# Optimization experiments

Measured on AMD Instinct MI355X. Metric: run time of the kernel, lower is better.

The kernel has to match this reference:

```python
import jax, jax.numpy as jnp
import numpy as np

N_NODES = 50000
N_EDGES = 800000
NODE_FEAT = 176
EDGE_FEAT = 4
HIDDEN = 64
LAYERS = 4
LN_EPS = 1e-5


def setup_inputs() -> dict:
    key = jax.random.key(0)
    ks = jax.random.split(key, 20)
    H, H2, Hh = HIDDEN, HIDDEN * 2, HIDDEN // 2
    inp = {
        "x": jax.random.normal(ks[0], (N_NODES, NODE_FEAT), jnp.float32),
        "edge_index": jax.random.randint(ks[1], (2, N_EDGES), 0, N_NODES, jnp.int64),
        "edge_attr": jax.random.normal(ks[2], (N_EDGES, EDGE_FEAT), jnp.float32),
        # input projection
        "in_w": jax.random.normal(ks[3], (NODE_FEAT, H), jnp.float32) * 0.05,
        "in_b": jnp.zeros((H,), jnp.float32),
        # per-layer GINEConv params (stacked over LAYERS)
        "edge_w": jax.random.normal(ks[4], (LAYERS, EDGE_FEAT, H), jnp.float32) * 0.1,
        "edge_b": jnp.zeros((LAYERS, H), jnp.float32),
        "mlp_w1": jax.random.normal(ks[5], (LAYERS, H, H2), jnp.float32) * 0.05,
        "mlp_b1": jnp.zeros((LAYERS, H2), jnp.float32),
        "mlp_w2": jax.random.normal(ks[6], (LAYERS, H2, H), jnp.float32) * 0.05,
        "mlp_b2": jnp.zeros((LAYERS, H), jnp.float32),
        "ln_g": jnp.ones((LAYERS, H), jnp.float32),
        "ln_b": jnp.zeros((LAYERS, H), jnp.float32),
        "reg_w1": jax.random.normal(ks[7], (H, Hh), jnp.float32) * 0.1,
        "reg_b1": jnp.zeros((Hh,), jnp.float32),
        "reg_w2": jax.random.normal(ks[8], (Hh, 1), jnp.float32) * 0.1,
        "reg_b2": jnp.zeros((1,), jnp.float32),
    }
    return inp


def _layernorm(z, g, b):
    mu = jnp.mean(z, axis=-1, keepdims=True)
    var = jnp.mean((z - mu) ** 2, axis=-1, keepdims=True)
    return g * (z - mu) * jax.lax.rsqrt(var + LN_EPS) + b


def reference(x, edge_index, edge_attr, in_w, in_b, edge_w, edge_b,
              mlp_w1, mlp_b1, mlp_w2, mlp_b2, ln_g, ln_b,
              reg_w1, reg_b1, reg_w2, reg_b2):
    src, dst = edge_index[0], edge_index[1]
    h = x @ in_w + in_b  # [N, H]
    for l in range(LAYERS):
        e = edge_attr @ edge_w[l] + edge_b[l]              # [E, H] edge projection
        msg = jax.nn.relu(h[src] + e)                      # gather + relu
        aggr = jax.ops.segment_sum(msg, dst, num_segments=h.shape[0])  # scatter-add
        z = h + aggr                                       # (1+eps)*x_i + aggr, eps=0
        z = jax.nn.relu(z @ mlp_w1[l] + mlp_b1[l]) @ mlp_w2[l] + mlp_b2[l]
        h = jax.nn.relu(_layernorm(z, ln_g[l], ln_b[l]))
    g = jnp.sum(h, axis=0)                                 # global_add_pool, single graph
    out = jax.nn.relu(g @ reg_w1 + reg_b1) @ reg_w2 + reg_b2
    return out.squeeze()
```

## Files before the change

### kernel.cpp

```cpp
#include <hip/hip_runtime.h>

#define N_NODES 50000
#define N_EDGES 800000
#define NODE_FEAT 176
#define HIDDEN 64
#define LN_EPS 1e-5f
#define SCAN_NB 49

typedef short bf16x8 __attribute__((ext_vector_type(8)));
typedef float f32x4 __attribute__((ext_vector_type(4)));
typedef long long ll2 __attribute__((ext_vector_type(2)));

__device__ __forceinline__ unsigned short f2bf(float f) {
    unsigned int u = __float_as_uint(f);
    u += 0x7FFFu + ((u >> 16) & 1u);
    return (unsigned short)(u >> 16);
}
__device__ __forceinline__ int pack2(float lo, float hi) {
    return (int)(((unsigned)f2bf(hi) << 16) | (unsigned)f2bf(lo));
}
__device__ __forceinline__ float bf2f(unsigned short s) {
    return __uint_as_float(((unsigned int)s) << 16);
}

#if __has_builtin(__builtin_amdgcn_cvt_pk_fp8_f32) && __has_builtin(__builtin_amdgcn_cvt_f32_fp8)
#define HW_FP8 1
#endif

__device__ __forceinline__ unsigned char f2fp8(float f) {
#ifdef HW_FP8
    return (unsigned char)(__builtin_amdgcn_cvt_pk_fp8_f32(f, f, 0, false) & 0xff);
#else
    unsigned u = __float_as_uint(f);
    unsigned s = (u >> 24) & 0x80u;
    float a = fabsf(f);
    if (a >= 448.f) return (unsigned char)(s | 0x7E);
    if (a < 0.0078125f) {
        int m = (int)fmaf(a, 512.0f, 0.5f);
        return (unsigned char)(s | (m > 7 ? 7 : m));
    }
    unsigned au = u & 0x7fffffffu;
    au += 0x7ffffu + ((au >> 20) & 1u);
    int e8 = (int)(au >> 23) - 120;
    if (e8 <= 0) {
        int m = (int)fmaf(__uint_as_float(au), 512.0f, 0.5f);
        return (unsigned char)(s | (m > 7 ? 7 : m));
    }
    if (e8 > 15) return (unsigned char)(s | 0x7E);
    return (unsigned char)(s | (e8 << 3) | ((au >> 20) & 7));
#endif
}
__device__ __forceinline__ float fp82f(int b) {
#ifdef HW_FP8
    return __builtin_amdgcn_cvt_f32_fp8(b & 0xff, 0);
#else
    int s = (b >> 7) & 1, e = (b >> 3) & 15, m = b & 7;
    float v = e ? __uint_as_float(((unsigned)(e + 120) << 23) | ((unsigned)m << 20))
                : (float)m * 0.001953125f;
    return s ? -v : v;
#endif
}

__device__ __forceinline__ float wave_sum64(float v) {
#pragma unroll
    for (int o = 32; o > 0; o >>= 1) v += __shfl_xor(v, o);
    return v;
}
__device__ __forceinline__ float sum16(float v) {
#pragma unroll
    for (int o = 8; o > 0; o >>= 1) v += __shfl_xor(v, o);
    return v;
}

__global__ __launch_bounds__(256) void k_wprep(const float* __restrict__ in_w,
                                               const float* __restrict__ w1,
                                               const float* __restrict__ w2,
                                               unsigned short* __restrict__ fin,
                                               unsigned short* __restrict__ f1,
                                               unsigned short* __restrict__ f2,
                                               int* __restrict__ cnt) {
    int t = blockIdx.x * 256 + threadIdx.x;
    if (t < N_NODES) cnt[t] = 0;
    if (t < 12288) {
        int e = t;
        int r = e & 7, lane = (e >> 3) & 63, j = (e >> 9) & 3, s = e >> 11;
        int k = s * 32 + ((lane >> 4) << 3) + r;
        int n = (j << 4) + (lane & 15);
        fin[e] = (k < NODE_FEAT) ? f2bf(in_w[k * 64 + n]) : (unsigned short)0;
    } else if (t < 12288 + 32768) {
        int e = t - 12288;
        int L = e >> 13, e2 = e & 8191;
        int r = e2 & 7, lane = (e2 >> 3) & 63, j = (e2 >> 9) & 7, s = (e2 >> 12) & 1;
        int k = s * 32 + ((lane >> 4) << 3) + r;
        int n = (j << 4) + (lane & 15);
        f1[e] = f2bf(w1[L * 8192 + k * 128 + n]);
    } else if (t < 12288 + 32768 + 32768) {
        int e = t - 45056;
        int L = e >> 13, e2 = e & 8191;
        int r = e2 & 7, lane = (e2 >> 3) & 63, j = (e2 >> 9) & 3, s = (e2 >> 11) & 3;
        int k = s * 32 + ((lane >> 4) << 3) + r;
        int n = (j << 4) + (lane & 15);
        f2[e] = f2bf(w2[L * 8192 + k * 64 + n]);
    }
}

__global__ __launch_bounds__(256) void k_inproj_mfma(const float* __restrict__ x,
                                                     const unsigned short* __restrict__ wfrag,
                                                     const float* __restrict__ in_b,
                                                     unsigned short* __restrict__ hb,
                                                     unsigned char* __restrict__ hf8) {
    __shared__ unsigned short lw[12288];
    const int tid = threadIdx.x;
    {
        const bf16x8* src = (const bf16x8*)wfrag;
        bf16x8* dst = (bf16x8*)lw;
        for (int i = tid; i < 1536; i += 256) dst[i] = src[i];
    }
    __syncthreads();
    const int wv = tid >> 6, lane = tid & 63;
    const int lrow = lane & 15, lgrp = lane >> 4;
    float ib[4];
#pragma unroll
    for (int j = 0; j < 4; ++j) ib[j] = in_b[16 * j + lrow];
    const int nwaves = gridDim.x * 4;
    for (int tile = blockIdx.x * 4 + wv; tile < 3125; tile += nwaves) {
        const int m0 = tile * 16;
        f32x4 acc[4];
#pragma unroll
        for (int j = 0; j < 4; ++j) acc[j] = (f32x4){ib[j], ib[j], ib[j], ib[j]};
#pragma unroll
        for (int s = 0; s < 6; ++s) {
            const int kbase = s * 32 + lgrp * 8;
            bf16x8 a;
            if (kbase < NODE_FEAT) {
                const float* p = x + (size_t)(m0 + lrow) * NODE_FEAT + kbase;
                float4 fa = *(const float4*)p;
                float4 fb = *(const float4*)(p + 4);
                a[0] = (short)f2bf(fa.x); a[1] = (short)f2bf(fa.y);
                a[2] = (short)f2bf(fa.z); a[3] = (short)f2bf(fa.w);
                a[4] = (short)f2bf(fb.x); a[5] = (short)f2bf(fb.y);
                a[6] = (short)f2bf(fb.z); a[7] = (short)f2bf(fb.w);
            } else {
                a = (bf16x8){0, 0, 0, 0, 0, 0, 0, 0};
            }
#pragma unroll
            for (int j = 0; j < 4; ++j) {
                bf16x8 b = *(const bf16x8*)&lw[((s * 4 + j) * 64 + lane) * 8];
                acc[j] = __builtin_amdgcn_mfma_f32_16x16x32_bf16(a, b, acc[j], 0, 0, 0);
            }
        }
#pragma unroll
        for (int j = 0; j < 4; ++j) {
            const int col = 16 * j + lrow;
#pragma unroll
            for (int r = 0; r < 4; ++r) {
                const int node = m0 + lgrp * 4 + r;
                float v = acc[j][r];
                __builtin_nontemporal_store(f2bf(v), &hb[(size_t)node * 64 + col]);
                hf8[(size_t)node * 64 + col] = f2fp8(v);
            }
        }
    }
}

__global__ __launch_bounds__(256) void k_hist(const int* __restrict__ ei,
                                              int* __restrict__ cnt,
                                              int* __restrict__ erank) {
    int e = blockIdx.x * 256 + threadIdx.x;
    if (e < N_EDGES) erank[e] = atomicAdd(&cnt[ei[N_EDGES + e]], 1);
}

__global__ __launch_bounds__(256) void k_scan_part(const int* __restrict__ cnt,
                                                   int* __restrict__ blksum) {
    const int b = blockIdx.x, t = threadIdx.x;
    const int base = b * 1024 + t * 4;
    int s = 0;
#pragma unroll
    for (int i = 0; i < 4; ++i) {
        int idx = base + i;
        if (idx < N_NODES) s += cnt[idx];
    }
#pragma unroll
    for (int o = 32; o > 0; o >>= 1) s += __shfl_xor(s, o);
    __shared__ int wt[4];
    if ((t & 63) == 0) wt[t >> 6] = s;
    __syncthreads();
    if (t == 0) blksum[b] = wt[0] + wt[1] + wt[2] + wt[3];
}

__global__ __launch_bounds__(64) void k_scan_top(const int* __restrict__ blksum,
                                                 int* __restrict__ blkoff,
                                                 int* __restrict__ row_last) {
    const int t = threadIdx.x;
    int v = (t < SCAN_NB) ? blksum[t] : 0;
    int incl = v;
#pragma unroll
    for (int o = 1; o < 64; o <<= 1) {
        int u = __shfl_up(incl, o);
        if (t >= o) incl += u;
    }
    if (t < SCAN_NB) blkoff[t] = incl - v;
    if (t == 63) row_last[0] = incl;
}

__global__ __launch_bounds__(256) void k_scan_add(const int* __restrict__ cnt,
                                                  const int* __restrict__ blkoff,
                                                  int* __restrict__ row_ptr) {
    const int b = blockIdx.x, t = threadIdx.x;
    const int base = b * 1024 + t * 4;
    int c[4];
    int tsum = 0;
#pragma unroll
    for (int i = 0; i < 4; ++i) {
        int idx = base + i;
        c[i] = (idx < N_NODES) ? cnt[idx] : 0;
        tsum += c[i];
    }
    int incl = tsum;
#pragma unroll
    for (int o = 1; o < 64; o <<= 1) {
        int u = __shfl_up(incl, o);
        if ((t & 63) >= o) incl += u;
    }
    __shared__ int wt[4];
    const int wv = t >> 6;
    if ((t & 63) == 63) wt[wv] = incl;
    __syncthreads();
    int run = blkoff[b] + (incl - tsum);
    for (int w = 0; w < wv; ++w) run += wt[w];
#pragma unroll
    for (int i = 0; i < 4; ++i) {
        int idx = base + i;
        if (idx < N_NODES) row_ptr[idx] = run;
        run += c[i];
    }
}

__global__ __launch_bounds__(256) void k_scatter(const int* __restrict__ ei,
                                                 const float4* __restrict__ ea,
                                                 const int* __restrict__ row_ptr,
                                                 const int* __restrict__ erank,
                                                 int4* __restrict__ rec) {
    int e = blockIdx.x * 256 + threadIdx.x;
    if (e >= N_EDGES) return;
    int d = ei[N_EDGES + e];
    float4 a = ea[e];
    int4 r;
    r.x = pack2(a.x, a.y);
    r.y = pack2(a.z, a.w);
    r.z = ei[e];
    r.w = 0;
    rec[row_ptr[d] + erank[e]] = r;
}

__global__ __launch_bounds__(256) void k_aggr(const unsigned short* __restrict__ hb_in,
                                              const unsigned char* __restrict__ hf8_in,
                                              unsigned short* __restrict__ zb,
                                              const int* __restrict__ row_ptr,
                                              const int4* __restrict__ rec,
                                              const float* __restrict__ ew,
                                              const float* __restrict__ eb) {
    const int wv = threadIdx.x >> 6, lane = threadIdx.x & 63;
    const int node = blockIdx.x * 4 + wv;
    const float ew0 = ew[0 * 64 + lane], ew1 = ew[1 * 64 + lane];
    const float ew2 = ew[2 * 64 + lane], ew3 = ew[3 * 64 + lane];
    const float ebl = eb[lane];
    const int beg = __builtin_amdgcn_readfirstlane(row_ptr[node]);
    const int end = __builtin_amdgcn_readfirstlane(row_ptr[node + 1]);
    float acc = bf2f(__builtin_nontemporal_load(&hb_in[(size_t)node * 64 + lane]));
    int i = beg;
    for (; i + 8 <= end; i += 8) {
        int d0[8], d1[8], sx[8];
#pragma unroll
        for (int t = 0; t < 8; ++t) {
            ll2 r = __builtin_nontemporal_load((const ll2*)(rec + i + t));
            d0[t] = __builtin_amdgcn_readfirstlane((int)(r[0] & 0xffffffffLL));
            d1[t] = __builtin_amdgcn_readfirstlane((int)(r[0] >> 32));
            sx[t] = __builtin_amdgcn_readfirstlane((int)(r[1] & 0xffffffffLL));
        }
        float gg[8];
#pragma unroll
        for (int t = 0; t < 8; ++t)
            gg[t] = fp82f(hf8_in[((size_t)sx[t] << 6) + lane]);
#pragma unroll
        for (int t = 0; t < 8; ++t) {
            float a0 = __uint_as_float((unsigned)d0[t] << 16);
            float a1 = __uint_as_float((unsigned)d0[t] & 0xffff0000u);
            float a2 = __uint_as_float((unsigned)d1[t] << 16);
            float a3 = __uint_as_float((unsigned)d1[t] & 0xffff0000u);
            float v = fmaf(a0, ew0, fmaf(a1, ew1, fmaf(a2, ew2, fmaf(a3, ew3, ebl))));
            acc += fmaxf(v + gg[t], 0.0f);
        }
    }
    if (i < end) {
        const int n = end - i;
        int d0[8], d1[8], sx[8];
#pragma unroll
        for (int t = 0; t < 8; ++t) {
            int idx = i + ((t < n) ? t : (n - 1));
            ll2 r = __builtin_nontemporal_load((const ll2*)(rec + idx));
            d0[t] = __builtin_amdgcn_readfirstlane((int)(r[0] & 0xffffffffLL));
            d1[t] = __builtin_amdgcn_readfirstlane((int)(r[0] >> 32));
            sx[t] = __builtin_amdgcn_readfirstlane((int)(r[1] & 0xffffffffLL));
        }
        float gg[8];
#pragma unroll
        for (int t = 0; t < 8; ++t)
            gg[t] = fp82f(hf8_in[((size_t)sx[t] << 6) + lane]);
#pragma unroll
        for (int t = 0; t < 8; ++t) {
            float m = (t < n) ? 1.0f : 0.0f;
            float a0 = __uint_as_float((unsigned)d0[t] << 16);
            float a1 = __uint_as_float((unsigned)d0[t] & 0xffff0000u);
            float a2 = __uint_as_float((unsigned)d1[t] << 16);
            float a3 = __uint_as_float((unsigned)d1[t] & 0xffff0000u);
            float v = fmaf(a0, ew0, fmaf(a1, ew1, fmaf(a2, ew2, fmaf(a3, ew3, ebl))));
            acc += m * fmaxf(v + gg[t], 0.0f);
        }
    }
    __builtin_nontemporal_store(f2bf(acc), &zb[(size_t)node * 64 + lane]);
}

__global__ __launch_bounds__(256) void k_mlp_mfma(const unsigned short* __restrict__ zb,
                                                  unsigned short* __restrict__ hb_out,
                                                  unsigned char* __restrict__ hf8_out,
                                                  const unsigned short* __restrict__ f1,
                                                  const unsigned short* __restrict__ f2,
                                                  const float* __restrict__ b1,
                                                  const float* __restrict__ b2,
                                                  const float* __restrict__ lng,
                                                  const float* __restrict__ lnb) {
    __shared__ unsigned short w1f[8192];
    __shared__ unsigned short w2f[8192];
    __shared__ unsigned short z1s[4][2048];
    const int tid = threadIdx.x;
    {
        const bf16x8* s1 = (const bf16x8*)f1;
        const bf16x8* s2 = (const bf16x8*)f2;
        bf16x8* d1 = (bf16x8*)w1f;
        bf16x8* d2 = (bf16x8*)w2f;
        for (int i = tid; i < 1024; i += 256) { d1[i] = s1[i]; d2[i] = s2[i]; }
    }
    __syncthreads();
    const int wv = tid >> 6, lane = tid & 63;
    const int lrow = lane & 15, lgrp = lane >> 4;
    unsigned short* zs = z1s[wv];
    float bb1[8], bb2[4], g4[4], be4[4];
#pragma unroll
    for (int j = 0; j < 8; ++j) bb1[j] = b1[16 * j + lrow];
#pragma unroll
    for (int j = 0; j < 4; ++j) {
        bb2[j] = b2[16 * j + lrow];
        g4[j] = lng[16 * j + lrow];
        be4[j] = lnb[16 * j + lrow];
    }
    const int nwaves = gridDim.x * 4;
    for (int tile = blockIdx.x * 4 + wv; tile < 3125; tile += nwaves) {
        const int m0 = tile * 16;
        f32x4 acc1[8];
#pragma unroll
        for (int j = 0; j < 8; ++j) acc1[j] = (f32x4){bb1[j], bb1[j], bb1[j], bb1[j]};
#pragma unroll
        for (int s = 0; s < 2; ++s) {
            const int kbase = s * 32 + lgrp * 8;
            bf16x8 a = *(const bf16x8*)&zb[(size_t)(m0 + lrow) * 64 + kbase];
#pragma unroll
            for (int j = 0; j < 8; ++j) {
                bf16x8 b = *(const bf16x8*)&w1f[((s * 8 + j) * 64 + lane) * 8];
                acc1[j] = __builtin_amdgcn_mfma_f32_16x16x32_bf16(a, b, acc1[j], 0, 0, 0);
            }
        }
#pragma unroll
        for (int j = 0; j < 8; ++j) {
            const int col = 16 * j + lrow;
#pragma unroll
            for (int r = 0; r < 4; ++r) {
                const int row = lgrp * 4 + r;
                const int idx = (row * 128 + col) ^ ((row & 7) << 3);
                zs[idx] = f2bf(fmaxf(acc1[j][r], 0.0f));
            }
        }
        f32x4 acc2[4];
#pragma unroll
        for (int j = 0; j < 4; ++j) acc2[j] = (f32x4){bb2[j], bb2[j], bb2[j], bb2[j]};
#pragma unroll
        for (int s = 0; s < 4; ++s) {
            const int kbase = s * 32 + lgrp * 8;
            const int idx = (lrow * 128 + kbase) ^ ((lrow & 7) << 3);
            bf16x8 a = *(const bf16x8*)&zs[idx];
#pragma unroll
            for (int j = 0; j < 4; ++j) {
                bf16x8 b = *(const bf16x8*)&w2f[((s * 4 + j) * 64 + lane) * 8];
                acc2[j] = __builtin_amdgcn_mfma_f32_16x16x32_bf16(a, b, acc2[j], 0, 0, 0);
            }
        }
#pragma unroll
        for (int r = 0; r < 4; ++r) {
            float sum = acc2[0][r] + acc2[1][r] + acc2[2][r] + acc2[3][r];
            sum = sum16(sum);
            const float mu = sum * (1.0f / 64.0f);
            float sq = 0.0f;
#pragma unroll
            for (int j = 0; j < 4; ++j) {
                float d = acc2[j][r] - mu;
                sq = fmaf(d, d, sq);
            }
            sq = sum16(sq);
            const float rstd = rsqrtf(sq * (1.0f / 64.0f) + LN_EPS);
            const int node = m0 + lgrp * 4 + r;
#pragma unroll
            for (int j = 0; j < 4; ++j) {
                const int col = 16 * j + lrow;
                float d = acc2[j][r] - mu;
                float hn = fmaxf(fmaf(g4[j] * d, rstd, be4[j]), 0.0f);
                __builtin_nontemporal_store(f2bf(hn), &hb_out[(size_t)node * 64 + col]);
                hf8_out[(size_t)node * 64 + col] = f2fp8(hn);
            }
        }
    }
}

__global__ __launch_bounds__(256) void k_pool(const unsigned short* __restrict__ hb,
                                              float* __restrict__ gpart) {
    __shared__ float red[256];
    const int tid = threadIdx.x;
    const int lane = tid & 63;
    float part = 0.0f;
    for (int i = blockIdx.x * 4 + (tid >> 6); i < N_NODES; i += gridDim.x * 4)
        part += bf2f(hb[(size_t)i * 64 + lane]);
    red[tid] = part;
    __syncthreads();
    if (tid < 64) {
        gpart[blockIdx.x * 64 + tid] = red[tid] + red[tid + 64] + red[tid + 128] + red[tid + 192];
    }
}

__global__ __launch_bounds__(64) void k_reg(const float* __restrict__ gpart,
                                            const float* __restrict__ w1,
                                            const float* __restrict__ b1,
                                            const float* __restrict__ w2,
                                            const float* __restrict__ b2,
                                            float* __restrict__ out) {
    const int j = threadIdx.x;
    float gj = 0.0f;
    for (int b = 0; b < 256; ++b) gj += gpart[b * 64 + j];
    __shared__ float gs[64];
    gs[j] = gj;
    __syncthreads();
    const int jm = j & 31;
    float acc = b1[jm];
#pragma unroll 8
    for (int k = 0; k < 64; ++k) {
        float gk = gs[k];
        acc = fmaf(gk, w1[k * 32 + jm], acc);
    }
    float contrib = (j < 32) ? fmaxf(acc, 0.0f) * w2[jm] : 0.0f;
    float s = wave_sum64(contrib);
    if (j == 0) out[0] = s + b2[0];
}

extern "C" void kernel_launch(void* const* d_in, const int* in_sizes, int n_in,
                              void* d_out, int out_size, void* d_ws, size_t ws_size,
                              hipStream_t stream) {
    const float* x      = (const float*)d_in[0];
    const int*   ei     = (const int*)d_in[1];
    const float* ea     = (const float*)d_in[2];
    const float* in_w   = (const float*)d_in[3];
    const float* in_b   = (const float*)d_in[4];
    const float* edge_w = (const float*)d_in[5];
    const float* edge_b = (const float*)d_in[6];
    const float* mlp_w1 = (const float*)d_in[7];
    const float* mlp_b1 = (const float*)d_in[8];
    const float* mlp_w2 = (const float*)d_in[9];
    const float* mlp_b2 = (const float*)d_in[10];
    const float* ln_g   = (const float*)d_in[11];
    const float* ln_b   = (const float*)d_in[12];
    const float* reg_w1 = (const float*)d_in[13];
    const float* reg_b1 = (const float*)d_in[14];
    const float* reg_w2 = (const float*)d_in[15];
    const float* reg_b2 = (const float*)d_in[16];

    char* ws = (char*)d_ws;
    unsigned short* hb0     = (unsigned short*)ws; ws += (size_t)N_NODES * 64 * 2;
    unsigned short* hb1     = (unsigned short*)ws; ws += (size_t)N_NODES * 64 * 2;
    unsigned short* zb      = (unsigned short*)ws; ws += (size_t)N_NODES * 64 * 2;
    unsigned char*  hf8_0   = (unsigned char*)ws;  ws += (size_t)N_NODES * 64;
    unsigned char*  hf8_1   = (unsigned char*)ws;  ws += (size_t)N_NODES * 64;
    int4*           rec     = (int4*)ws;           ws += (size_t)N_EDGES * 16;
    unsigned short* fin     = (unsigned short*)ws; ws += 12288 * 2;
    unsigned short* f1      = (unsigned short*)ws; ws += 32768 * 2;
    unsigned short* f2      = (unsigned short*)ws; ws += 32768 * 2;
    int*            erank   = (int*)ws;            ws += (size_t)N_EDGES * 4;
    int*            row_ptr = (int*)ws;            ws += (size_t)(N_NODES + 1) * 4;
    int*            cnt     = (int*)ws;            ws += (size_t)N_NODES * 4;
    int*            blksum  = (int*)ws;            ws += SCAN_NB * 4;
    int*            blkoff  = (int*)ws;            ws += SCAN_NB * 4;
    float*          gpart   = (float*)ws;          ws += 256 * 64 * 4;
    float*          outf    = (float*)d_out;

    const int eb_blocks = (N_EDGES + 255) / 256;

    k_wprep<<<304, 256, 0, stream>>>(in_w, mlp_w1, mlp_w2, fin, f1, f2, cnt);

    k_hist<<<eb_blocks, 256, 0, stream>>>(ei, cnt, erank);
    k_scan_part<<<SCAN_NB, 256, 0, stream>>>(cnt, blksum);
    k_scan_top<<<1, 64, 0, stream>>>(blksum, blkoff, row_ptr + N_NODES);
    k_scan_add<<<SCAN_NB, 256, 0, stream>>>(cnt, blkoff, row_ptr);
    k_scatter<<<eb_blocks, 256, 0, stream>>>(ei, (const float4*)ea, row_ptr, erank, rec);

    k_inproj_mfma<<<512, 256, 0, stream>>>(x, fin, in_b, hb0, hf8_0);

    unsigned short* hbA = hb0;
    unsigned short* hbB = hb1;
    unsigned char*  hfA = hf8_0;
    unsigned char*  hfB = hf8_1;
    for (int l = 0; l < 4; ++l) {
        k_aggr<<<N_NODES / 4, 256, 0, stream>>>(hbA, hfA, zb, row_ptr, rec,
                                                edge_w + l * 4 * 64,
                                                edge_b + l * 64);
        k_mlp_mfma<<<768, 256, 0, stream>>>(zb, hbB, hfB,
                                            f1 + l * 8192, f2 + l * 8192,
                                            mlp_b1 + l * 128, mlp_b2 + l * 64,
                                            ln_g + l * 64, ln_b + l * 64);
        unsigned short* tb = hbA; hbA = hbB; hbB = tb;
        unsigned char*  tf = hfA; hfA = hfB; hfB = tf;
    }

    k_pool<<<256, 256, 0, stream>>>(hbA, gpart);
    k_reg<<<1, 64, 0, stream>>>(gpart, reg_w1, reg_b1, reg_w2, reg_b2, outf);
}
```

Baseline: 276.0 us.

## Prefetch edge records in aggregation, fold scan-top into scan-add, grid-stride histogram

After: 284.3 us. +3.0%, slower.

```diff
diff --git a/kernel.cpp b/kernel.cpp
--- a/kernel.cpp
+++ b/kernel.cpp
@@ -166,8 +166,16 @@
 __global__ __launch_bounds__(256) void k_hist(const int* __restrict__ ei,
                                               int* __restrict__ cnt,
                                               int* __restrict__ erank) {
-    int e = blockIdx.x * 256 + threadIdx.x;
-    if (e < N_EDGES) erank[e] = atomicAdd(&cnt[ei[N_EDGES + e]], 1);
+    const int tid = blockIdx.x * 256 + threadIdx.x;
+#pragma unroll
+    for (int k = 0; k < 6; ++k) {
+        int e = tid + k * 131072;
+        erank[e] = atomicAdd(&cnt[ei[N_EDGES + e]], 1);
+    }
+    {
+        int e = tid + 6 * 131072;
+        if (e < N_EDGES) erank[e] = atomicAdd(&cnt[ei[N_EDGES + e]], 1);
+    }
 }
 
 __global__ __launch_bounds__(256) void k_scan_part(const int* __restrict__ cnt,
@@ -188,25 +196,23 @@
     if (t == 0) blksum[b] = wt[0] + wt[1] + wt[2] + wt[3];
 }
 
-__global__ __launch_bounds__(64) void k_scan_top(const int* __restrict__ blksum,
-                                                 int* __restrict__ blkoff,
-                                                 int* __restrict__ row_last) {
-    const int t = threadIdx.x;
-    int v = (t < SCAN_NB) ? blksum[t] : 0;
-    int incl = v;
-#pragma unroll
-    for (int o = 1; o < 64; o <<= 1) {
-        int u = __shfl_up(incl, o);
-        if (t >= o) incl += u;
-    }
-    if (t < SCAN_NB) blkoff[t] = incl - v;
-    if (t == 63) row_last[0] = incl;
-}
-
 __global__ __launch_bounds__(256) void k_scan_add(const int* __restrict__ cnt,
-                                                  const int* __restrict__ blkoff,
+                                                  const int* __restrict__ blksum,
                                                   int* __restrict__ row_ptr) {
     const int b = blockIdx.x, t = threadIdx.x;
+    __shared__ int boff_s;
+    if (t < 64) {
+        int v = (t < SCAN_NB) ? blksum[t] : 0;
+        int incl = v;
+#pragma unroll
+        for (int o = 1; o < 64; o <<= 1) {
+            int u = __shfl_up(incl, o);
+            if (t >= o) incl += u;
+        }
+        if (t == b) boff_s = incl - v;
+        if (b == 0 && t == 63) row_ptr[N_NODES] = incl;
+    }
+    __syncthreads();
     const int base = b * 1024 + t * 4;
     int c[4];
     int tsum = 0;
@@ -226,7 +232,7 @@
     const int wv = t >> 6;
     if ((t & 63) == 63) wt[wv] = incl;
     __syncthreads();
-    int run = blkoff[b] + (incl - tsum);
+    int run = boff_s + (incl - tsum);
     for (int w = 0; w < wv; ++w) run += wt[w];
 #pragma unroll
     for (int i = 0; i < 4; ++i) {
@@ -268,15 +274,27 @@
     const int beg = __builtin_amdgcn_readfirstlane(row_ptr[node]);
     const int end = __builtin_amdgcn_readfirstlane(row_ptr[node + 1]);
     float acc = bf2f(__builtin_nontemporal_load(&hb_in[(size_t)node * 64 + lane]));
+    const int nb = (end - beg) >> 3;
     int i = beg;
-    for (; i + 8 <= end; i += 8) {
+    ll2 ra[8];
+    if (nb > 0) {
+#pragma unroll
+        for (int t = 0; t < 8; ++t)
+            ra[t] = __builtin_nontemporal_load((const ll2*)(rec + i + t));
+    }
+    for (int k = 0; k < nb; ++k) {
+        ll2 rb[8];
+        if (k + 1 < nb) {
+#pragma unroll
+            for (int t = 0; t < 8; ++t)
+                rb[t] = __builtin_nontemporal_load((const ll2*)(rec + i + 8 + t));
+        }
         int d0[8], d1[8], sx[8];
 #pragma unroll
         for (int t = 0; t < 8; ++t) {
-            ll2 r = __builtin_nontemporal_load((const ll2*)(rec + i + t));
-            d0[t] = __builtin_amdgcn_readfirstlane((int)(r[0] & 0xffffffffLL));
-            d1[t] = __builtin_amdgcn_readfirstlane((int)(r[0] >> 32));
-            sx[t] = __builtin_amdgcn_readfirstlane((int)(r[1] & 0xffffffffLL));
+            d0[t] = __builtin_amdgcn_readfirstlane((int)(ra[t][0] & 0xffffffffLL));
+            d1[t] = __builtin_amdgcn_readfirstlane((int)(ra[t][0] >> 32));
+            sx[t] = __builtin_amdgcn_readfirstlane((int)(ra[t][1] & 0xffffffffLL));
         }
         float gg[8];
 #pragma unroll
@@ -291,6 +309,11 @@
             float v = fmaf(a0, ew0, fmaf(a1, ew1, fmaf(a2, ew2, fmaf(a3, ew3, ebl))));
             acc += fmaxf(v + gg[t], 0.0f);
         }
+        if (k + 1 < nb) {
+#pragma unroll
+            for (int t = 0; t < 8; ++t) ra[t] = rb[t];
+        }
+        i += 8;
     }
     if (i < end) {
         const int n = end - i;
@@ -494,7 +517,6 @@
     int*            row_ptr = (int*)ws;            ws += (size_t)(N_NODES + 1) * 4;
     int*            cnt     = (int*)ws;            ws += (size_t)N_NODES * 4;
     int*            blksum  = (int*)ws;            ws += SCAN_NB * 4;
-    int*            blkoff  = (int*)ws;            ws += SCAN_NB * 4;
     float*          gpart   = (float*)ws;          ws += 256 * 64 * 4;
     float*          outf    = (float*)d_out;
 
@@ -502,10 +524,9 @@
 
     k_wprep<<<304, 256, 0, stream>>>(in_w, mlp_w1, mlp_w2, fin, f1, f2, cnt);
 
-    k_hist<<<eb_blocks, 256, 0, stream>>>(ei, cnt, erank);
+    k_hist<<<512, 256, 0, stream>>>(ei, cnt, erank);
     k_scan_part<<<SCAN_NB, 256, 0, stream>>>(cnt, blksum);
-    k_scan_top<<<1, 64, 0, stream>>>(blksum, blkoff, row_ptr + N_NODES);
-    k_scan_add<<<SCAN_NB, 256, 0, stream>>>(cnt, blkoff, row_ptr);
+    k_scan_add<<<SCAN_NB, 256, 0, stream>>>(cnt, blksum, row_ptr);
     k_scatter<<<eb_blocks, 256, 0, stream>>>(ei, (const float4*)ea, row_ptr, erank, rec);
 
     k_inproj_mfma<<<512, 256, 0, stream>>>(x, fin, in_b, hb0, hf8_0);
```
